# Kernel optimization log

Hardware: AMD Instinct MI355X
Metric: run time of the kernel (lower is better)

## Reference

```python
import jax, jax.numpy as jnp
import numpy as np

N, E, IN = 50000, 800000, 64
HC, FC1, FC2, FC3, OUT = 96, 256, 128, 64, 8
EPS = 1e-5


def setup_inputs() -> dict:
    key = jax.random.key(0)
    ks = jax.random.split(key, 24)
    def lin(k, fi, fo):
        # kaiming_uniform with relu gain: bound = sqrt(6/fi)
        b = np.sqrt(6.0 / fi)
        return jax.random.uniform(k, (fi, fo), jnp.float32, -b, b)
    inp = {
        'x': jax.random.normal(ks[0], (N, IN), jnp.float32),
        'edge_index': jax.random.randint(ks[1], (2, E), 0, N, jnp.int64),
        'w1': lin(ks[2], IN, HC), 'b1': jnp.zeros((HC,), jnp.float32),
        'g1': jax.random.uniform(ks[3], (HC,), jnp.float32, 0.5, 1.5), 'be1': jax.random.normal(ks[4], (HC,), jnp.float32) * 0.1,
        'w2': lin(ks[5], HC, HC), 'b2': jnp.zeros((HC,), jnp.float32),
        'g2': jax.random.uniform(ks[6], (HC,), jnp.float32, 0.5, 1.5), 'be2': jax.random.normal(ks[7], (HC,), jnp.float32) * 0.1,
        'w3': lin(ks[8], HC, HC), 'b3': jnp.zeros((HC,), jnp.float32),
        'g3': jax.random.uniform(ks[9], (HC,), jnp.float32, 0.5, 1.5), 'be3': jax.random.normal(ks[10], (HC,), jnp.float32) * 0.1,
        'lw1': lin(ks[11], HC, FC1), 'lb1': jnp.zeros((FC1,), jnp.float32),
        'lw2': lin(ks[12], FC1, FC2), 'lb2': jnp.zeros((FC2,), jnp.float32),
        'lw3': lin(ks[13], FC2, FC3), 'lb3': jnp.zeros((FC3,), jnp.float32),
        'lw4': lin(ks[14], FC3, OUT), 'lb4': jnp.zeros((OUT,), jnp.float32),
    }
    return inp


def _gcn(x, w, b, src, dst, norm):
    # GCNConv: out[dst] += norm_e * (x @ w)[src]; then + bias
    h = x @ w
    msg = h[src] * norm[:, None]
    return jax.ops.segment_sum(msg, dst, num_segments=N) + b


def _bn_eval(x, g, be):
    # eval-mode BatchNorm1d with running_mean=0, running_var=1
    return x / jnp.sqrt(1.0 + EPS) * g + be


def reference(x, edge_index, w1, b1, g1, be1, w2, b2, g2, be2, w3, b3, g3, be3,
              lw1, lb1, lw2, lb2, lw3, lb3, lw4, lb4):
    loops = jnp.arange(N, dtype=edge_index.dtype)
    src = jnp.concatenate([edge_index[0], loops])
    dst = jnp.concatenate([edge_index[1], loops])
    deg = jax.ops.segment_sum(jnp.ones_like(src, jnp.float32), dst, num_segments=N)
    dinv = jax.lax.rsqrt(deg)  # deg >= 1 due to self loops
    norm = dinv[src] * dinv[dst]

    h = jax.nn.relu(_bn_eval(_gcn(x, w1, b1, src, dst, norm), g1, be1))
    h = jax.nn.relu(_bn_eval(_gcn(h, w2, b2, src, dst, norm), g2, be2))
    h = jax.nn.relu(_bn_eval(_gcn(h, w3, b3, src, dst, norm), g3, be3))
    h = jax.nn.relu(h @ lw1 + lb1)
    h = jax.nn.relu(h @ lw2 + lb2)
    h = jax.nn.relu(h @ lw3 + lb3)
    return h @ lw4 + lb4
```

## Files before the change

### kernel.cpp

```cpp
#include <hip/hip_runtime.h>


#define GN 50000
#define GE 800000
#define NPART 98
#define PSLOT 9216
#define CHK 2048

typedef __attribute__((ext_vector_type(8))) short bf16x8;
typedef __attribute__((ext_vector_type(4))) float floatx4;

__device__ __forceinline__ float ar1_b2f(unsigned short h) {
    return __uint_as_float(((unsigned)h) << 16);
}
__device__ __forceinline__ unsigned short ar1_f2b(float f) {
    unsigned u = __float_as_uint(f);
    u = u + 0x7FFFu + ((u >> 16) & 1u);
    return (unsigned short)(u >> 16);
}

__device__ __forceinline__ int ar1_det64(const int* ei) {
    int l = (int)threadIdx.x & 63;
    int nz = 0;
#pragma unroll
    for (int k = 0; k < 4; k++)
        nz += (ei[2 * (l + 64 * k) + 1] != 0) ? 1 : 0;
#pragma unroll
    for (int o = 1; o < 64; o <<= 1)
        nz += __shfl_xor(nz, o, 64);
    return (nz < 8) ? 1 : 0;
}
__device__ __forceinline__ int ar1_detf32(const unsigned short* xw) {
    int l = (int)threadIdx.x & 63;
    int c = 0;
#pragma unroll
    for (int k = 0; k < 4; k++) {
        unsigned short w = xw[2 * (l + 64 * k)];
        int ex = (w >> 7) & 0xFF;
        if (w == 0 || (ex >= 90 && ex <= 150)) c++;
    }
#pragma unroll
    for (int o = 1; o < 64; o <<= 1)
        c += __shfl_xor(c, o, 64);
    return (c > 200) ? 0 : 1;
}

struct PackAll {
    const void* src[7];
    unsigned short* dst[7];
    int K[7], M[7], start[8];
};
struct SmallCvt {
    const void* src[4];
    float* dst[4];
    int n[4];
    const void* gb[9];
    float* ss[6];
};

__global__ __launch_bounds__(256)
void Arthur1_16458314678864_kernel(PackAll pa, SmallCvt sc,
                                   const int* __restrict__ ei,
                                   const unsigned short* __restrict__ xw,
                                   int* flagI, int* flagF,
                                   int* __restrict__ gcur,
                                   unsigned int* __restrict__ pairs) {
    int b = (int)blockIdx.x;
    int tid = (int)threadIdx.x;
    if (b < 391) {
        __shared__ int cnt[NPART], base[NPART], cur[NPART];
        for (int i = tid; i < NPART; i += 256) { cnt[i] = 0; cur[i] = 0; }
        int is64 = ar1_det64(ei);
        __syncthreads();
        int e0 = b * CHK;
        unsigned pk[8]; int q[8];
#pragma unroll
        for (int k = 0; k < 8; k++) {
            int e = e0 + k * 256 + tid;
            q[k] = -1; pk[k] = 0;
            if (e < GE) {
                int s = is64 ? ei[2 * e] : ei[e];
                int d = is64 ? ei[2 * (GE + e)] : ei[GE + e];
                if ((unsigned)s < (unsigned)GN && (unsigned)d < (unsigned)GN) {
                    int qq = d >> 9;
                    q[k] = qq;
                    pk[k] = (unsigned)s | ((unsigned)(d & 511) << 17);
                    atomicAdd(&cnt[qq], 1);
                }
            }
        }
        __syncthreads();
        for (int i = tid; i < NPART; i += 256)
            base[i] = (cnt[i] > 0) ? atomicAdd(&gcur[i], cnt[i]) : 0;
        __syncthreads();
#pragma unroll
        for (int k = 0; k < 8; k++) {
            if (q[k] >= 0) {
                int r = base[q[k]] + atomicAdd(&cur[q[k]], 1);
                if (r < PSLOT) pairs[(size_t)q[k] * PSLOT + r] = pk[k];
            }
        }
    } else if (b < 436) {
        int f = ar1_detf32(xw);
        int frag_g = (b - 391) * 4 + (tid >> 6);
        if (frag_g >= 178) return;
        int w = 0;
        while (w < 6 && frag_g >= pa.start[w + 1]) w++;
        int frag = frag_g - pa.start[w];
        int K = pa.K[w], M = pa.M[w];
        int lane = tid & 63;
        int nch = K >> 5;
        int t = frag / nch, c = frag - t * nch;
        int n = t * 16 + (lane & 15);
        int k0 = c * 32 + (lane >> 4) * 8;
        unsigned short* o = pa.dst[w] + ((size_t)frag * 64 + lane) * 8;
        for (int j = 0; j < 8; j++) {
            unsigned short v = 0;
            if (n < M) {
                int idx = (k0 + j) * M + n;
                v = f ? ar1_f2b(((const float*)pa.src[w])[idx])
                      : ((const unsigned short*)pa.src[w])[idx];
            }
            o[j] = v;
        }
    } else {
        int f = ar1_detf32(xw);
        int i64 = ar1_det64(ei);
        if (tid == 0) { flagI[0] = i64; flagF[0] = f; }
        const float C = 0.9999950000374997f;
        for (int s = 0; s < 4; s++) {
            for (int i = tid; i < sc.n[s]; i += 256) {
                float v = f ? ((const float*)sc.src[s])[i]
                            : ar1_b2f(((const unsigned short*)sc.src[s])[i]);
                sc.dst[s][i] = v;
            }
        }
        for (int k = 0; k < 3; k++) {
            for (int i = tid; i < 96; i += 256) {
                float bb, g, be;
                if (f) {
                    bb = ((const float*)sc.gb[3 * k + 0])[i];
                    g  = ((const float*)sc.gb[3 * k + 1])[i];
                    be = ((const float*)sc.gb[3 * k + 2])[i];
                } else {
                    bb = ar1_b2f(((const unsigned short*)sc.gb[3 * k + 0])[i]);
                    g  = ar1_b2f(((const unsigned short*)sc.gb[3 * k + 1])[i]);
                    be = ar1_b2f(((const unsigned short*)sc.gb[3 * k + 2])[i]);
                }
                sc.ss[2 * k + 0][i] = C * g;
                sc.ss[2 * k + 1][i] = bb * C * g + be;
            }
        }
    }
}

__global__ __launch_bounds__(256)
void ar1_csr(const unsigned int* __restrict__ pairs, const int* __restrict__ gcur,
             int* __restrict__ csr, int* __restrict__ indeg,
             int* __restrict__ offs, float* __restrict__ dinv) {
    __shared__ int ncnt[512], pre[512], cur[512], psum[16], red[256];
    int p = (int)blockIdx.x, tid = (int)threadIdx.x;
    red[tid] = (tid < p && tid < NPART) ? gcur[tid] : 0;
    __syncthreads();
    for (int o = 128; o > 0; o >>= 1) {
        if (tid < o) red[tid] += red[tid + o];
        __syncthreads();
    }
    int gbase = red[0];
    int cntE = gcur[p];
    if (cntE > PSLOT) cntE = PSLOT;
    for (int i = tid; i < 512; i += 256) ncnt[i] = 0;
    __syncthreads();
    const unsigned int* pp = pairs + (size_t)p * PSLOT;
    for (int i = tid; i < cntE; i += 256) atomicAdd(&ncnt[pp[i] >> 17], 1);
    __syncthreads();
    if (tid < 16) {
        int s = 0;
        for (int j = tid * 32; j < tid * 32 + 32; j++) { pre[j] = s; s += ncnt[j]; }
        psum[tid] = s;
    }
    __syncthreads();
    if (tid == 0) {
        int s = 0;
        for (int j = 0; j < 16; j++) { int t = psum[j]; psum[j] = s; s += t; }
    }
    __syncthreads();
    if (tid < 16)
        for (int j = tid * 32; j < tid * 32 + 32; j++) pre[j] += psum[tid];
    __syncthreads();
    for (int j = tid; j < 512; j += 256) {
        cur[j] = pre[j];
        int node = p * 512 + j;
        if (node < GN) {
            indeg[node] = ncnt[j];
            offs[node] = gbase + pre[j];
            dinv[node] = rsqrtf((float)(ncnt[j] + 1));
        }
    }
    __syncthreads();
    for (int i = tid; i < cntE; i += 256) {
        unsigned v = pp[i];
        int r = atomicAdd(&cur[v >> 17], 1);
        csr[gbase + r] = (int)(v & 0x1FFFFu);
    }
}

__global__ __launch_bounds__(1024, 8)
void ar1_ag64g(const void* __restrict__ Xv, const int* __restrict__ offs,
               const int* __restrict__ indeg, const int* __restrict__ csr,
               const float* __restrict__ dinv, const int* __restrict__ flagF,
               const unsigned short* __restrict__ Bp,
               const float* __restrict__ scale, const float* __restrict__ shift,
               unsigned short* __restrict__ C) {
    __shared__ unsigned short AL[16 * 72];
    int tid = (int)threadIdx.x, wv = tid >> 6, lane = tid & 63;
    int nb = (int)blockIdx.x * 16;
    int node = nb + wv;
    int chunk = lane & 7, eslot = lane >> 3;
    int f = flagF[0];
    const unsigned short* X16 = (const unsigned short*)Xv;
    const float* X32 = (const float*)Xv;
    float di = dinv[node];
    int off = offs[node], cnt = indeg[node];

    float acc[8];
#pragma unroll
    for (int j = 0; j < 8; j++) acc[j] = 0.f;

    for (int base = 0; base < cnt; base += 16) {
        int ss[2]; float ww[2];
#pragma unroll
        for (int k = 0; k < 2; k++) {
            int e = base + k * 8 + eslot;
            int s = node; float w = 0.f;
            if (e < cnt) {
                s = csr[off + e];
                if ((unsigned)s >= (unsigned)GN) s = node;
                w = dinv[s] * di;
            }
            ss[k] = s; ww[k] = w;
        }
#pragma unroll
        for (int k = 0; k < 2; k++) {
            float hv[8];
            if (f) {
                floatx4 a = *((const floatx4*)(X32 + (size_t)ss[k] * 64 + chunk * 8));
                floatx4 b = *((const floatx4*)(X32 + (size_t)ss[k] * 64 + chunk * 8 + 4));
#pragma unroll
                for (int j = 0; j < 4; j++) { hv[j] = a[j]; hv[4 + j] = b[j]; }
            } else {
                bf16x8 h = *((const bf16x8*)(X16 + (size_t)ss[k] * 64 + chunk * 8));
#pragma unroll
                for (int j = 0; j < 8; j++) hv[j] = ar1_b2f((unsigned short)h[j]);
            }
#pragma unroll
            for (int j = 0; j < 8; j++) acc[j] += ww[k] * hv[j];
        }
    }
#pragma unroll
    for (int j = 0; j < 8; j++) {
        acc[j] += __shfl_xor(acc[j], 8, 64);
        acc[j] += __shfl_xor(acc[j], 16, 64);
        acc[j] += __shfl_xor(acc[j], 32, 64);
    }
    if (eslot == 0) {
        float hv[8];
        if (f) {
            floatx4 a = *((const floatx4*)(X32 + (size_t)node * 64 + chunk * 8));
            floatx4 b = *((const floatx4*)(X32 + (size_t)node * 64 + chunk * 8 + 4));
#pragma unroll
            for (int j = 0; j < 4; j++) { hv[j] = a[j]; hv[4 + j] = b[j]; }
        } else {
            bf16x8 h = *((const bf16x8*)(X16 + (size_t)node * 64 + chunk * 8));
#pragma unroll
            for (int j = 0; j < 8; j++) hv[j] = ar1_b2f((unsigned short)h[j]);
        }
        bf16x8 o;
#pragma unroll
        for (int j = 0; j < 8; j++)
            o[j] = (short)ar1_f2b(acc[j] + di * di * hv[j]);
        *((bf16x8*)(AL + (size_t)wv * 72 + chunk * 8)) = o;
    }
    __syncthreads();

    if (wv < 6) {
        int m = lane & 15, quad = lane >> 4, t = wv;
        floatx4 g = (floatx4){0.f, 0.f, 0.f, 0.f};
#pragma unroll
        for (int c = 0; c < 2; c++) {
            bf16x8 a = *((const bf16x8*)(AL + (size_t)m * 72 + c * 32 + quad * 8));
            bf16x8 bfr = *((const bf16x8*)(Bp + ((size_t)(t * 2 + c) * 64 + lane) * 8));
            g = __builtin_amdgcn_mfma_f32_16x16x32_bf16(a, bfr, g, 0, 0, 0);
        }
#pragma unroll
        for (int r = 0; r < 4; r++) {
            int row = nb + quad * 4 + r;
            int col = t * 16 + m;
            float v = g[r] * scale[col] + shift[col];
            C[(size_t)row * 96 + col] = ar1_f2b(fmaxf(v, 0.f));
        }
    }
}

__global__ __launch_bounds__(1024, 8)
void ar1_ag96g(const unsigned short* __restrict__ H, const int* __restrict__ offs,
               const int* __restrict__ indeg, const int* __restrict__ csr,
               const float* __restrict__ dinv,
               const unsigned short* __restrict__ Bp,
               const float* __restrict__ scale, const float* __restrict__ shift,
               unsigned short* __restrict__ C) {
    __shared__ unsigned short AL[16 * 104];
    int tid = (int)threadIdx.x, wv = tid >> 6, lane = tid & 63;
    int nb = (int)blockIdx.x * 16;
    int node = nb + wv;
    int chunk = lane % 12, eslot = lane / 12;
    int active = (lane < 48) ? 1 : 0;
    float di = dinv[node];
    int off = offs[node], cnt = indeg[node];

    float acc[8];
#pragma unroll
    for (int j = 0; j < 8; j++) acc[j] = 0.f;

    if (active) {
        for (int base = 0; base < cnt; base += 16) {
            int ss[4]; float ww[4]; bf16x8 hh[4];
#pragma unroll
            for (int k = 0; k < 4; k++) {
                int e = base + k * 4 + eslot;
                int s = node; float w = 0.f;
                if (e < cnt) {
                    s = csr[off + e];
                    if ((unsigned)s >= (unsigned)GN) s = node;
                    w = dinv[s] * di;
                }
                ss[k] = s; ww[k] = w;
            }
#pragma unroll
            for (int k = 0; k < 4; k++)
                hh[k] = *((const bf16x8*)(H + (size_t)ss[k] * 96 + chunk * 8));
#pragma unroll
            for (int k = 0; k < 4; k++)
#pragma unroll
                for (int j = 0; j < 8; j++)
                    acc[j] += ww[k] * ar1_b2f((unsigned short)hh[k][j]);
        }
    }
#pragma unroll
    for (int j = 0; j < 8; j++) {
        float a1 = __shfl(acc[j], lane + 12, 64);
        float a2 = __shfl(acc[j], lane + 24, 64);
        float a3 = __shfl(acc[j], lane + 36, 64);
        acc[j] += a1 + a2 + a3;
    }
    if (lane < 12) {
        bf16x8 hs = *((const bf16x8*)(H + (size_t)node * 96 + chunk * 8));
        bf16x8 o;
#pragma unroll
        for (int j = 0; j < 8; j++)
            o[j] = (short)ar1_f2b(acc[j] + di * di * ar1_b2f((unsigned short)hs[j]));
        *((bf16x8*)(AL + (size_t)wv * 104 + chunk * 8)) = o;
    }
    __syncthreads();

    if (wv < 6) {
        int m = lane & 15, quad = lane >> 4, t = wv;
        floatx4 g = (floatx4){0.f, 0.f, 0.f, 0.f};
#pragma unroll
        for (int c = 0; c < 3; c++) {
            bf16x8 a = *((const bf16x8*)(AL + (size_t)m * 104 + c * 32 + quad * 8));
            bf16x8 bfr = *((const bf16x8*)(Bp + ((size_t)(t * 3 + c) * 64 + lane) * 8));
            g = __builtin_amdgcn_mfma_f32_16x16x32_bf16(a, bfr, g, 0, 0, 0);
        }
#pragma unroll
        for (int r = 0; r < 4; r++) {
            int row = nb + quad * 4 + r;
            int col = t * 16 + m;
            float v = g[r] * scale[col] + shift[col];
            C[(size_t)row * 96 + col] = ar1_f2b(fmaxf(v, 0.f));
        }
    }
}

__global__ __launch_bounds__(256, 8)
void ar1_agg96(const unsigned short* __restrict__ H, const int* __restrict__ offs,
               const int* __restrict__ indeg, const int* __restrict__ csr,
               const float* __restrict__ dinv, unsigned short* __restrict__ Out) {
    int wv = (int)threadIdx.x >> 6, lane = (int)threadIdx.x & 63;
    int node = (int)blockIdx.x * 4 + wv;
    if (node >= GN) return;
    int chunk = lane % 12;
    int eslot = lane / 12;
    int active = (lane < 48) ? 1 : 0;
    float di = dinv[node];
    int off = offs[node], cnt = indeg[node];

    float acc[8];
#pragma unroll
    for (int j = 0; j < 8; j++) acc[j] = 0.f;

    if (active) {
        for (int base = 0; base < cnt; base += 16) {
            int ss[4]; float ww[4]; bf16x8 hh[4];
#pragma unroll
            for (int k = 0; k < 4; k++) {
                int e = base + k * 4 + eslot;
                int s = node; float w = 0.f;
                if (e < cnt) {
                    s = csr[off + e];
                    if ((unsigned)s >= (unsigned)GN) s = node;
                    w = dinv[s] * di;
                }
                ss[k] = s; ww[k] = w;
            }
#pragma unroll
            for (int k = 0; k < 4; k++)
                hh[k] = *((const bf16x8*)(H + (size_t)ss[k] * 96 + chunk * 8));
#pragma unroll
            for (int k = 0; k < 4; k++)
#pragma unroll
                for (int j = 0; j < 8; j++)
                    acc[j] += ww[k] * ar1_b2f((unsigned short)hh[k][j]);
        }
    }
#pragma unroll
    for (int j = 0; j < 8; j++) {
        float a1 = __shfl(acc[j], lane + 12, 64);
        float a2 = __shfl(acc[j], lane + 24, 64);
        float a3 = __shfl(acc[j], lane + 36, 64);
        acc[j] += a1 + a2 + a3;
    }
    if (lane < 12) {
        bf16x8 hs = *((const bf16x8*)(H + (size_t)node * 96 + chunk * 8));
#pragma unroll
        for (int j = 0; j < 8; j++) {
            float v = acc[j] + di * di * ar1_b2f((unsigned short)hs[j]);
            Out[(size_t)node * 96 + chunk * 8 + j] = ar1_f2b(v);
        }
    }
}

__global__ __launch_bounds__(256, 2)
void ar1_mlp2(const unsigned short* __restrict__ A,
              const unsigned short* __restrict__ b2w,
              const float* __restrict__ sc3, const float* __restrict__ sh3,
              const unsigned short* __restrict__ b3,
              const unsigned short* __restrict__ b4,
              const unsigned short* __restrict__ b5,
              const unsigned short* __restrict__ b6,
              const float* __restrict__ lb0, const float* __restrict__ lb1,
              const float* __restrict__ lb2, const float* __restrict__ lb3,
              void* __restrict__ out, const int* __restrict__ f32out) {
    __shared__ unsigned short SH[16896 + 13312];
    unsigned short* H1 = SH;
    unsigned short* H0 = SH + 16896;
    unsigned short* H2 = SH + 16896;
    unsigned short* H3 = SH + 16896 + 8704;
    int tid = (int)threadIdx.x, wv = tid >> 6, lane = tid & 63;
    int m = lane & 15, quad = lane >> 4;
    int mb = (int)blockIdx.x * 64 + wv * 16;
    int lwv = wv * 16;

    {
        int arow = mb + m; if (arow >= GN) arow = GN - 1;
        const unsigned short* Ap = A + (size_t)arow * 96 + quad * 8;
        floatx4 acc[6];
#pragma unroll
        for (int t = 0; t < 6; t++) acc[t] = (floatx4){0.f, 0.f, 0.f, 0.f};
        for (int c = 0; c < 3; c++) {
            bf16x8 a = *((const bf16x8*)(Ap + c * 32));
#pragma unroll
            for (int t = 0; t < 6; t++) {
                bf16x8 b = *((const bf16x8*)(b2w + ((size_t)(t * 3 + c) * 64 + lane) * 8));
                acc[t] = __builtin_amdgcn_mfma_f32_16x16x32_bf16(a, b, acc[t], 0, 0, 0);
            }
        }
#pragma unroll
        for (int t = 0; t < 6; t++)
#pragma unroll
            for (int r = 0; r < 4; r++) {
                int lr = lwv + quad * 4 + r, col = t * 16 + m;
                float v = acc[t][r] * sc3[col] + sh3[col];
                H0[lr * 104 + col] = ar1_f2b(fmaxf(v, 0.f));
            }
    }
    {
        const unsigned short* Hp = H0 + (size_t)(lwv + m) * 104 + quad * 8;
        floatx4 acc[16];
#pragma unroll
        for (int t = 0; t < 16; t++) acc[t] = (floatx4){0.f, 0.f, 0.f, 0.f};
        for (int c = 0; c < 3; c++) {
            bf16x8 a = *((const bf16x8*)(Hp + c * 32));
#pragma unroll
            for (int t = 0; t < 16; t++) {
                bf16x8 b = *((const bf16x8*)(b3 + ((size_t)(t * 3 + c) * 64 + lane) * 8));
                acc[t] = __builtin_amdgcn_mfma_f32_16x16x32_bf16(a, b, acc[t], 0, 0, 0);
            }
        }
#pragma unroll
        for (int t = 0; t < 16; t++)
#pragma unroll
            for (int r = 0; r < 4; r++) {
                int lr = lwv + quad * 4 + r, col = t * 16 + m;
                H1[lr * 264 + col] = ar1_f2b(fmaxf(acc[t][r] + lb0[col], 0.f));
            }
    }
    {
        const unsigned short* Hp = H1 + (size_t)(lwv + m) * 264 + quad * 8;
        floatx4 acc[8];
#pragma unroll
        for (int t = 0; t < 8; t++) acc[t] = (floatx4){0.f, 0.f, 0.f, 0.f};
        for (int c = 0; c < 8; c++) {
            bf16x8 a = *((const bf16x8*)(Hp + c * 32));
#pragma unroll
            for (int t = 0; t < 8; t++) {
                bf16x8 b = *((const bf16x8*)(b4 + ((size_t)(t * 8 + c) * 64 + lane) * 8));
                acc[t] = __builtin_amdgcn_mfma_f32_16x16x32_bf16(a, b, acc[t], 0, 0, 0);
            }
        }
#pragma unroll
        for (int t = 0; t < 8; t++)
#pragma unroll
            for (int r = 0; r < 4; r++) {
                int lr = lwv + quad * 4 + r, col = t * 16 + m;
                H2[lr * 136 + col] = ar1_f2b(fmaxf(acc[t][r] + lb1[col], 0.f));
            }
    }
    {
        const unsigned short* Hp = H2 + (size_t)(lwv + m) * 136 + quad * 8;
        floatx4 acc[4];
#pragma unroll
        for (int t = 0; t < 4; t++) acc[t] = (floatx4){0.f, 0.f, 0.f, 0.f};
        for (int c = 0; c < 4; c++) {
            bf16x8 a = *((const bf16x8*)(Hp + c * 32));
#pragma unroll
            for (int t = 0; t < 4; t++) {
                bf16x8 b = *((const bf16x8*)(b5 + ((size_t)(t * 4 + c) * 64 + lane) * 8));
                acc[t] = __builtin_amdgcn_mfma_f32_16x16x32_bf16(a, b, acc[t], 0, 0, 0);
            }
        }
#pragma unroll
        for (int t = 0; t < 4; t++)
#pragma unroll
            for (int r = 0; r < 4; r++) {
                int lr = lwv + quad * 4 + r, col = t * 16 + m;
                H3[lr * 72 + col] = ar1_f2b(fmaxf(acc[t][r] + lb2[col], 0.f));
            }
    }
    {
        const unsigned short* Hp = H3 + (size_t)(lwv + m) * 72 + quad * 8;
        floatx4 acc = (floatx4){0.f, 0.f, 0.f, 0.f};
        for (int c = 0; c < 2; c++) {
            bf16x8 a = *((const bf16x8*)(Hp + c * 32));
            bf16x8 b = *((const bf16x8*)(b6 + ((size_t)c * 64 + lane) * 8));
            acc = __builtin_amdgcn_mfma_f32_16x16x32_bf16(a, b, acc, 0, 0, 0);
        }
        int wf32 = f32out[0];
#pragma unroll
        for (int r = 0; r < 4; r++) {
            int row = mb + quad * 4 + r;
            if (row < GN && m < 8) {
                float v = acc[r] + lb3[m];
                if (wf32) ((float*)out)[(size_t)row * 8 + m] = v;
                else ((unsigned short*)out)[(size_t)row * 8 + m] = ar1_f2b(v);
            }
        }
    }
}

extern "C" void kernel_launch(void* const* d_in, const int* in_sizes, int n_in,
                              void* d_out, int out_size, void* d_ws, size_t ws_size,
                              hipStream_t stream) {
    (void)in_sizes; (void)n_in; (void)out_size;

    char* p = (char*)d_ws;
    unsigned short* bufA = (unsigned short*)p; p += (size_t)GN * 96 * 2;
    unsigned short* bufB = (unsigned short*)p; p += (size_t)GN * 96 * 2;
    unsigned short* bufC = (unsigned short*)p; p += (size_t)GN * 96 * 2;
    unsigned int* pairs = (unsigned int*)p; p += (size_t)NPART * PSLOT * 4;
    int* indeg  = (int*)p;    p += (size_t)GN * 4;
    int* offs   = (int*)p;    p += (size_t)GN * 4;
    float* dinv = (float*)p;  p += (size_t)GN * 4;
    int* csr    = (int*)p;    p += (size_t)GE * 4;
    int* gcur   = (int*)p;    p += 1024;
    int* flagI  = (int*)p;    p += 1024;
    int* flagF  = (int*)p;    p += 1024;
    unsigned short* bpArena = (unsigned short*)p; p += 91136 * 2;
    float* fArena = (float*)p; p += 2048 * 4;
    size_t need = (size_t)(p - (char*)d_ws);
    if (ws_size < need) {
        hipMemsetAsync(d_out, 0x41, (size_t)GN * 8 * 2, stream);
        return;
    }

    unsigned short* bp[7];
    int bpn[7] = {6144, 9216, 9216, 24576, 32768, 8192, 1024};
    {
        unsigned short* q = bpArena;
        for (int i = 0; i < 7; i++) { bp[i] = q; q += bpn[i]; }
    }

    float* lb[4]; float* ss[6];
    {
        float* q = fArena;
        int ln[4] = {256, 128, 64, 8};
        for (int i = 0; i < 4; i++) { lb[i] = q; q += ln[i]; }
        for (int i = 0; i < 6; i++) { ss[i] = q; q += 96; }
    }

    const int* ei = (const int*)d_in[1];
    const unsigned short* xw = (const unsigned short*)d_in[0];

    hipMemsetAsync(gcur, 0, NPART * 4, stream);
    {
        PackAll pa;
        int wsrc[7] = {2, 6, 10, 14, 16, 18, 20};
        int Ks[7] = {64, 96, 96, 96, 256, 128, 64};
        int Ms[7] = {96, 96, 96, 256, 128, 64, 8};
        int cum = 0;
        for (int i = 0; i < 7; i++) {
            pa.src[i] = d_in[wsrc[i]]; pa.dst[i] = bp[i];
            pa.K[i] = Ks[i]; pa.M[i] = Ms[i];
            pa.start[i] = cum;
            cum += (Ms[i] + 15) / 16 * (Ks[i] / 32);
        }
        pa.start[7] = cum;
        SmallCvt sc;
        int lsrc[4] = {15, 17, 19, 21};
        int ln[4] = {256, 128, 64, 8};
        for (int i = 0; i < 4; i++) { sc.src[i] = d_in[lsrc[i]]; sc.dst[i] = lb[i]; sc.n[i] = ln[i]; }
        int gsrc[9] = {3, 4, 5, 7, 8, 9, 11, 12, 13};
        for (int i = 0; i < 9; i++) sc.gb[i] = d_in[gsrc[i]];
        for (int i = 0; i < 6; i++) sc.ss[i] = ss[i];
        Arthur1_16458314678864_kernel<<<437, 256, 0, stream>>>(
            pa, sc, ei, xw, flagI, flagF, gcur, pairs);
    }
    ar1_csr<<<NPART, 256, 0, stream>>>(pairs, gcur, csr, indeg, offs, dinv);

    const int GB = (GN + 63) / 64;
    const int AB = GN / 4;
    const int FB = GN / 16;

    ar1_ag64g<<<FB, 1024, 0, stream>>>(d_in[0], offs, indeg, csr, dinv, flagF,
                                       bp[0], ss[0], ss[1], bufA);
    ar1_ag96g<<<FB, 1024, 0, stream>>>(bufA, offs, indeg, csr, dinv,
                                       bp[1], ss[2], ss[3], bufB);
    ar1_agg96<<<AB, 256, 0, stream>>>(bufB, offs, indeg, csr, dinv, bufC);

    ar1_mlp2<<<GB, 256, 0, stream>>>(bufC, bp[2], ss[4], ss[5],
                                     bp[3], bp[4], bp[5], bp[6],
                                     lb[0], lb[1], lb[2], lb[3], d_out, flagF);
}
```

Measured before the change: 292.8 us.

## Fuse third-layer aggregation with W3 GEMM and MLP head into one kernel

Merges the layer-3 neighbor aggregation and the MLP kernel into one 1024-thread kernel that handles 16 nodes per block. Each wave aggregates one node into shared memory, then waves split the output column tiles of each GEMM stage, with block barriers between stages. This drops the intermediate global buffer and one launch, in exchange for idle waves during the narrower GEMM stages, several barriers per block, and weights reloaded per 16-node block.

```diff
diff --git a/kernel.cpp b/kernel.cpp
--- a/kernel.cpp
+++ b/kernel.cpp
@@ -382,185 +382,162 @@
     }
 }
 
-__global__ __launch_bounds__(256, 8)
-void ar1_agg96(const unsigned short* __restrict__ H, const int* __restrict__ offs,
+__global__ __launch_bounds__(1024, 8)
+void ar1_agmlp(const unsigned short* __restrict__ H, const int* __restrict__ offs,
                const int* __restrict__ indeg, const int* __restrict__ csr,
-               const float* __restrict__ dinv, unsigned short* __restrict__ Out) {
-    int wv = (int)threadIdx.x >> 6, lane = (int)threadIdx.x & 63;
-    int node = (int)blockIdx.x * 4 + wv;
-    if (node >= GN) return;
-    int chunk = lane % 12;
-    int eslot = lane / 12;
-    int active = (lane < 48) ? 1 : 0;
-    float di = dinv[node];
-    int off = offs[node], cnt = indeg[node];
-
-    float acc[8];
-#pragma unroll
-    for (int j = 0; j < 8; j++) acc[j] = 0.f;
-
-    if (active) {
-        for (int base = 0; base < cnt; base += 16) {
-            int ss[4]; float ww[4]; bf16x8 hh[4];
-#pragma unroll
-            for (int k = 0; k < 4; k++) {
-                int e = base + k * 4 + eslot;
-                int s = node; float w = 0.f;
-                if (e < cnt) {
-                    s = csr[off + e];
-                    if ((unsigned)s >= (unsigned)GN) s = node;
-                    w = dinv[s] * di;
+               const float* __restrict__ dinv,
+               const unsigned short* __restrict__ b2w,
+               const float* __restrict__ sc3, const float* __restrict__ sh3,
+               const unsigned short* __restrict__ b3,
+               const unsigned short* __restrict__ b4,
+               const unsigned short* __restrict__ b5,
+               const unsigned short* __restrict__ b6,
+               const float* __restrict__ lb0, const float* __restrict__ lb1,
+               const float* __restrict__ lb2, const float* __restrict__ lb3,
+               void* __restrict__ out, const int* __restrict__ f32out) {
+    __shared__ unsigned short AL[16 * 104];
+    __shared__ unsigned short H0[16 * 104];
+    __shared__ unsigned short H1[16 * 264];
+    __shared__ unsigned short H2[16 * 136];
+    __shared__ unsigned short H3[16 * 72];
+    int tid = (int)threadIdx.x, wv = tid >> 6, lane = tid & 63;
+    int nb = (int)blockIdx.x * 16;
+    int node = nb + wv;
+    int m = lane & 15, quad = lane >> 4;
+
+    {
+        int chunk = lane % 12, eslot = lane / 12;
+        int active = (lane < 48) ? 1 : 0;
+        float di = dinv[node];
+        int off = offs[node], cnt = indeg[node];
+        float acc[8];
+#pragma unroll
+        for (int j = 0; j < 8; j++) acc[j] = 0.f;
+        if (active) {
+            for (int base = 0; base < cnt; base += 16) {
+                int ss[4]; float ww[4]; bf16x8 hh[4];
+#pragma unroll
+                for (int k = 0; k < 4; k++) {
+                    int e = base + k * 4 + eslot;
+                    int s = node; float w = 0.f;
+                    if (e < cnt) {
+                        s = csr[off + e];
+                        if ((unsigned)s >= (unsigned)GN) s = node;
+                        w = dinv[s] * di;
+                    }
+                    ss[k] = s; ww[k] = w;
                 }
-                ss[k] = s; ww[k] = w;
-            }
-#pragma unroll
-            for (int k = 0; k < 4; k++)
-                hh[k] = *((const bf16x8*)(H + (size_t)ss[k] * 96 + chunk * 8));
-#pragma unroll
-            for (int k = 0; k < 4; k++)
-#pragma unroll
-                for (int j = 0; j < 8; j++)
-                    acc[j] += ww[k] * ar1_b2f((unsigned short)hh[k][j]);
-        }
-    }
-#pragma unroll
-    for (int j = 0; j < 8; j++) {
-        float a1 = __shfl(acc[j], lane + 12, 64);
-        float a2 = __shfl(acc[j], lane + 24, 64);
-        float a3 = __shfl(acc[j], lane + 36, 64);
-        acc[j] += a1 + a2 + a3;
-    }
-    if (lane < 12) {
-        bf16x8 hs = *((const bf16x8*)(H + (size_t)node * 96 + chunk * 8));
+#pragma unroll
+                for (int k = 0; k < 4; k++)
+                    hh[k] = *((const bf16x8*)(H + (size_t)ss[k] * 96 + chunk * 8));
+#pragma unroll
+                for (int k = 0; k < 4; k++)
+#pragma unroll
+                    for (int j = 0; j < 8; j++)
+                        acc[j] += ww[k] * ar1_b2f((unsigned short)hh[k][j]);
+            }
+        }
 #pragma unroll
         for (int j = 0; j < 8; j++) {
-            float v = acc[j] + di * di * ar1_b2f((unsigned short)hs[j]);
-            Out[(size_t)node * 96 + chunk * 8 + j] = ar1_f2b(v);
-        }
-    }
-}
-
-__global__ __launch_bounds__(256, 2)
-void ar1_mlp2(const unsigned short* __restrict__ A,
-              const unsigned short* __restrict__ b2w,
-              const float* __restrict__ sc3, const float* __restrict__ sh3,
-              const unsigned short* __restrict__ b3,
-              const unsigned short* __restrict__ b4,
-              const unsigned short* __restrict__ b5,
-              const unsigned short* __restrict__ b6,
-              const float* __restrict__ lb0, const float* __restrict__ lb1,
-              const float* __restrict__ lb2, const float* __restrict__ lb3,
-              void* __restrict__ out, const int* __restrict__ f32out) {
-    __shared__ unsigned short SH[16896 + 13312];
-    unsigned short* H1 = SH;
-    unsigned short* H0 = SH + 16896;
-    unsigned short* H2 = SH + 16896;
-    unsigned short* H3 = SH + 16896 + 8704;
-    int tid = (int)threadIdx.x, wv = tid >> 6, lane = tid & 63;
-    int m = lane & 15, quad = lane >> 4;
-    int mb = (int)blockIdx.x * 64 + wv * 16;
-    int lwv = wv * 16;
+            float a1 = __shfl(acc[j], lane + 12, 64);
+            float a2 = __shfl(acc[j], lane + 24, 64);
+            float a3 = __shfl(acc[j], lane + 36, 64);
+            acc[j] += a1 + a2 + a3;
+        }
+        if (lane < 12) {
+            bf16x8 hs = *((const bf16x8*)(H + (size_t)node * 96 + chunk * 8));
+            bf16x8 o;
+#pragma unroll
+            for (int j = 0; j < 8; j++)
+                o[j] = (short)ar1_f2b(acc[j] + di * di * ar1_b2f((unsigned short)hs[j]));
+            *((bf16x8*)(AL + (size_t)wv * 104 + chunk * 8)) = o;
+        }
+    }
+    __syncthreads();
+
+    if (wv < 6) {
+        int t = wv;
+        floatx4 g = (floatx4){0.f, 0.f, 0.f, 0.f};
+#pragma unroll
+        for (int c = 0; c < 3; c++) {
+            bf16x8 a = *((const bf16x8*)(AL + (size_t)m * 104 + c * 32 + quad * 8));
+            bf16x8 bfr = *((const bf16x8*)(b2w + ((size_t)(t * 3 + c) * 64 + lane) * 8));
+            g = __builtin_amdgcn_mfma_f32_16x16x32_bf16(a, bfr, g, 0, 0, 0);
+        }
+#pragma unroll
+        for (int r = 0; r < 4; r++) {
+            int col = t * 16 + m;
+            float v = g[r] * sc3[col] + sh3[col];
+            H0[(quad * 4 + r) * 104 + col] = ar1_f2b(fmaxf(v, 0.f));
+        }
+    }
+    __syncthreads();
 
     {
-        int arow = mb + m; if (arow >= GN) arow = GN - 1;
-        const unsigned short* Ap = A + (size_t)arow * 96 + quad * 8;
-        floatx4 acc[6];
-#pragma unroll
-        for (int t = 0; t < 6; t++) acc[t] = (floatx4){0.f, 0.f, 0.f, 0.f};
+        int t = wv;
+        floatx4 g = (floatx4){0.f, 0.f, 0.f, 0.f};
+#pragma unroll
         for (int c = 0; c < 3; c++) {
-            bf16x8 a = *((const bf16x8*)(Ap + c * 32));
-#pragma unroll
-            for (int t = 0; t < 6; t++) {
-                bf16x8 b = *((const bf16x8*)(b2w + ((size_t)(t * 3 + c) * 64 + lane) * 8));
-                acc[t] = __builtin_amdgcn_mfma_f32_16x16x32_bf16(a, b, acc[t], 0, 0, 0);
-            }
-        }
-#pragma unroll
-        for (int t = 0; t < 6; t++)
-#pragma unroll
-            for (int r = 0; r < 4; r++) {
-                int lr = lwv + quad * 4 + r, col = t * 16 + m;
-                float v = acc[t][r] * sc3[col] + sh3[col];
-                H0[lr * 104 + col] = ar1_f2b(fmaxf(v, 0.f));
-            }
-    }
-    {
-        const unsigned short* Hp = H0 + (size_t)(lwv + m) * 104 + quad * 8;
-        floatx4 acc[16];
-#pragma unroll
-        for (int t = 0; t < 16; t++) acc[t] = (floatx4){0.f, 0.f, 0.f, 0.f};
-        for (int c = 0; c < 3; c++) {
-            bf16x8 a = *((const bf16x8*)(Hp + c * 32));
-#pragma unroll
-            for (int t = 0; t < 16; t++) {
-                bf16x8 b = *((const bf16x8*)(b3 + ((size_t)(t * 3 + c) * 64 + lane) * 8));
-                acc[t] = __builtin_amdgcn_mfma_f32_16x16x32_bf16(a, b, acc[t], 0, 0, 0);
-            }
-        }
-#pragma unroll
-        for (int t = 0; t < 16; t++)
-#pragma unroll
-            for (int r = 0; r < 4; r++) {
-                int lr = lwv + quad * 4 + r, col = t * 16 + m;
-                H1[lr * 264 + col] = ar1_f2b(fmaxf(acc[t][r] + lb0[col], 0.f));
-            }
-    }
-    {
-        const unsigned short* Hp = H1 + (size_t)(lwv + m) * 264 + quad * 8;
-        floatx4 acc[8];
-#pragma unroll
-        for (int t = 0; t < 8; t++) acc[t] = (floatx4){0.f, 0.f, 0.f, 0.f};
+            bf16x8 a = *((const bf16x8*)(H0 + (size_t)m * 104 + c * 32 + quad * 8));
+            bf16x8 bfr = *((const bf16x8*)(b3 + ((size_t)(t * 3 + c) * 64 + lane) * 8));
+            g = __builtin_amdgcn_mfma_f32_16x16x32_bf16(a, bfr, g, 0, 0, 0);
+        }
+#pragma unroll
+        for (int r = 0; r < 4; r++) {
+            int col = t * 16 + m;
+            H1[(quad * 4 + r) * 264 + col] = ar1_f2b(fmaxf(g[r] + lb0[col], 0.f));
+        }
+    }
+    __syncthreads();
+
+    if (wv < 8) {
+        int t = wv;
+        floatx4 g = (floatx4){0.f, 0.f, 0.f, 0.f};
+#pragma unroll
         for (int c = 0; c < 8; c++) {
-            bf16x8 a = *((const bf16x8*)(Hp + c * 32));
-#pragma unroll
-            for (int t = 0; t < 8; t++) {
-                bf16x8 b = *((const bf16x8*)(b4 + ((size_t)(t * 8 + c) * 64 + lane) * 8));
-                acc[t] = __builtin_amdgcn_mfma_f32_16x16x32_bf16(a, b, acc[t], 0, 0, 0);
-            }
-        }
-#pragma unroll
-        for (int t = 0; t < 8; t++)
-#pragma unroll
-            for (int r = 0; r < 4; r++) {
-                int lr = lwv + quad * 4 + r, col = t * 16 + m;
-                H2[lr * 136 + col] = ar1_f2b(fmaxf(acc[t][r] + lb1[col], 0.f));
-            }
-    }
-    {
-        const unsigned short* Hp = H2 + (size_t)(lwv + m) * 136 + quad * 8;
-        floatx4 acc[4];
-#pragma unroll
-        for (int t = 0; t < 4; t++) acc[t] = (floatx4){0.f, 0.f, 0.f, 0.f};
+            bf16x8 a = *((const bf16x8*)(H1 + (size_t)m * 264 + c * 32 + quad * 8));
+            bf16x8 bfr = *((const bf16x8*)(b4 + ((size_t)(t * 8 + c) * 64 + lane) * 8));
+            g = __builtin_amdgcn_mfma_f32_16x16x32_bf16(a, bfr, g, 0, 0, 0);
+        }
+#pragma unroll
+        for (int r = 0; r < 4; r++) {
+            int col = t * 16 + m;
+            H2[(quad * 4 + r) * 136 + col] = ar1_f2b(fmaxf(g[r] + lb1[col], 0.f));
+        }
+    }
+    __syncthreads();
+
+    if (wv < 4) {
+        int t = wv;
+        floatx4 g = (floatx4){0.f, 0.f, 0.f, 0.f};
+#pragma unroll
         for (int c = 0; c < 4; c++) {
-            bf16x8 a = *((const bf16x8*)(Hp + c * 32));
-#pragma unroll
-            for (int t = 0; t < 4; t++) {
-                bf16x8 b = *((const bf16x8*)(b5 + ((size_t)(t * 4 + c) * 64 + lane) * 8));
-                acc[t] = __builtin_amdgcn_mfma_f32_16x16x32_bf16(a, b, acc[t], 0, 0, 0);
-            }
-        }
-#pragma unroll
-        for (int t = 0; t < 4; t++)
-#pragma unroll
-            for (int r = 0; r < 4; r++) {
-                int lr = lwv + quad * 4 + r, col = t * 16 + m;
-                H3[lr * 72 + col] = ar1_f2b(fmaxf(acc[t][r] + lb2[col], 0.f));
-            }
-    }
-    {
-        const unsigned short* Hp = H3 + (size_t)(lwv + m) * 72 + quad * 8;
-        floatx4 acc = (floatx4){0.f, 0.f, 0.f, 0.f};
+            bf16x8 a = *((const bf16x8*)(H2 + (size_t)m * 136 + c * 32 + quad * 8));
+            bf16x8 bfr = *((const bf16x8*)(b5 + ((size_t)(t * 4 + c) * 64 + lane) * 8));
+            g = __builtin_amdgcn_mfma_f32_16x16x32_bf16(a, bfr, g, 0, 0, 0);
+        }
+#pragma unroll
+        for (int r = 0; r < 4; r++) {
+            int col = t * 16 + m;
+            H3[(quad * 4 + r) * 72 + col] = ar1_f2b(fmaxf(g[r] + lb2[col], 0.f));
+        }
+    }
+    __syncthreads();
+
+    if (wv == 0) {
+        floatx4 g = (floatx4){0.f, 0.f, 0.f, 0.f};
+#pragma unroll
         for (int c = 0; c < 2; c++) {
-            bf16x8 a = *((const bf16x8*)(Hp + c * 32));
-            bf16x8 b = *((const bf16x8*)(b6 + ((size_t)c * 64 + lane) * 8));
-            acc = __builtin_amdgcn_mfma_f32_16x16x32_bf16(a, b, acc, 0, 0, 0);
+            bf16x8 a = *((const bf16x8*)(H3 + (size_t)m * 72 + c * 32 + quad * 8));
+            bf16x8 bfr = *((const bf16x8*)(b6 + ((size_t)c * 64 + lane) * 8));
+            g = __builtin_amdgcn_mfma_f32_16x16x32_bf16(a, bfr, g, 0, 0, 0);
         }
         int wf32 = f32out[0];
 #pragma unroll
         for (int r = 0; r < 4; r++) {
-            int row = mb + quad * 4 + r;
-            if (row < GN && m < 8) {
-                float v = acc[r] + lb3[m];
+            int row = nb + quad * 4 + r;
+            if (m < 8) {
+                float v = g[r] + lb3[m];
                 if (wf32) ((float*)out)[(size_t)row * 8 + m] = v;
                 else ((unsigned short*)out)[(size_t)row * 8 + m] = ar1_f2b(v);
             }
@@ -576,7 +553,6 @@
     char* p = (char*)d_ws;
     unsigned short* bufA = (unsigned short*)p; p += (size_t)GN * 96 * 2;
     unsigned short* bufB = (unsigned short*)p; p += (size_t)GN * 96 * 2;
-    unsigned short* bufC = (unsigned short*)p; p += (size_t)GN * 96 * 2;
     unsigned int* pairs = (unsigned int*)p; p += (size_t)NPART * PSLOT * 4;
     int* indeg  = (int*)p;    p += (size_t)GN * 4;
     int* offs   = (int*)p;    p += (size_t)GN * 4;
@@ -637,17 +613,14 @@
     }
     ar1_csr<<<NPART, 256, 0, stream>>>(pairs, gcur, csr, indeg, offs, dinv);
 
-    const int GB = (GN + 63) / 64;
-    const int AB = GN / 4;
     const int FB = GN / 16;
 
     ar1_ag64g<<<FB, 1024, 0, stream>>>(d_in[0], offs, indeg, csr, dinv, flagF,
                                        bp[0], ss[0], ss[1], bufA);
     ar1_ag96g<<<FB, 1024, 0, stream>>>(bufA, offs, indeg, csr, dinv,
                                        bp[1], ss[2], ss[3], bufB);
-    ar1_agg96<<<AB, 256, 0, stream>>>(bufB, offs, indeg, csr, dinv, bufC);
-
-    ar1_mlp2<<<GB, 256, 0, stream>>>(bufC, bp[2], ss[4], ss[5],
-                                     bp[3], bp[4], bp[5], bp[6],
-                                     lb[0], lb[1], lb[2], lb[3], d_out, flagF);
-}
+    ar1_agmlp<<<FB, 1024, 0, stream>>>(bufB, offs, indeg, csr, dinv,
+                                       bp[2], ss[4], ss[5],
+                                       bp[3], bp[4], bp[5], bp[6],
+                                       lb[0], lb[1], lb[2], lb[3], d_out, flagF);
+}
```

Result: no change. 292.0 us (-0.3%).
